# Optimization experiments

Measured on AMD Instinct MI355X. Metric: run time of the kernel, lower is better.

Reference implementation:

```python
import jax, jax.numpy as jnp
import numpy as np
import math

C = 256
GROUPS = 32
EPS = 1e-5

def setup_inputs() -> dict:
    key = jax.random.key(0)
    ks = jax.random.split(key, 11)
    B, H, W = 8, 64, 64
    s = 1.0 / math.sqrt(C)
    return {
        "x": jax.random.normal(ks[0], (B, C, H, W), dtype=jnp.float32),
        "gamma": jnp.ones((C,), jnp.float32),
        "beta": jnp.zeros((C,), jnp.float32),
        "wq": jax.random.normal(ks[1], (C, C), jnp.float32) * s,
        "bq": jnp.zeros((C,), jnp.float32),
        "wk": jax.random.normal(ks[2], (C, C), jnp.float32) * s,
        "bk": jnp.zeros((C,), jnp.float32),
        "wv": jax.random.normal(ks[3], (C, C), jnp.float32) * s,
        "bv": jnp.zeros((C,), jnp.float32),
        "wp": jax.random.normal(ks[4], (C, C), jnp.float32) * s,
        "bp": jnp.zeros((C,), jnp.float32),
    }

def _group_norm(x, gamma, beta):
    B, Cc, H, W = x.shape
    xg = x.reshape(B, GROUPS, Cc // GROUPS, H, W)
    mu = xg.mean(axis=(2, 3, 4), keepdims=True)
    var = xg.var(axis=(2, 3, 4), keepdims=True)
    xn = ((xg - mu) * jax.lax.rsqrt(var + EPS)).reshape(B, Cc, H, W)
    return xn * gamma[None, :, None, None] + beta[None, :, None, None]

def reference(x, gamma, beta, wq, bq, wk, bk, wv, bv, wp, bp):
    B, Cc, H, W = x.shape
    T = H * W
    h = _group_norm(x, gamma, beta)           # (B,C,H,W)
    hf = h.reshape(B, Cc, T)                  # (B,C,T)
    # 1x1 convs = per-pixel linear maps over channels
    q = jnp.einsum('oc,bct->bto', wq, hf) + bq           # (B,T,C)
    k = jnp.einsum('oc,bct->bot', wk, hf) + bk[:, None]  # (B,C,T)
    v = jnp.einsum('oc,bct->bto', wv, hf) + bv           # (B,T,C)
    scores = jnp.einsum('btc,bcs->bts', q, k) / math.sqrt(Cc)
    attn = jax.nn.softmax(scores, axis=-1)    # (B,T,T)
    z = jnp.einsum('bts,bsc->btc', attn, v)   # (B,T,C)
    zf = z.transpose(0, 2, 1)                 # (B,C,T)
    proj = jnp.einsum('oc,bct->bot', wp, zf) + bp[:, None]
    return x + proj.reshape(B, Cc, H, W)
```

## Files before the change

kernel.cpp:

```cpp
#include <hip/hip_runtime.h>


typedef unsigned short u16;
typedef __attribute__((ext_vector_type(8))) short short8;
typedef __attribute__((ext_vector_type(4))) float f32x4;

#define MFMA16(a, b, c) __builtin_amdgcn_mfma_f32_16x16x32_bf16((a), (b), (c), 0, 0, 0)

#define GLL16(g, l)                                                            \
  __builtin_amdgcn_global_load_lds(                                            \
      (const __attribute__((address_space(1))) void*)(g),                      \
      (__attribute__((address_space(3))) void*)(l), 16, 0, 0)

__device__ __forceinline__ u16 f2bf(float f) {
  union { float f; unsigned u; } v; v.f = f;
  unsigned u = v.u;
  return (u16)((u + 0x7FFFu + ((u >> 16) & 1u)) >> 16);
}

__global__ __launch_bounds__(256) void conv_w(const float* __restrict__ s0,
                                              const float* __restrict__ s1,
                                              const float* __restrict__ s2,
                                              const float* __restrict__ s3,
                                              u16* __restrict__ dst) {
  const int m = blockIdx.y;
  const float* s = (m == 0) ? s0 : (m == 1) ? s1 : (m == 2) ? s2 : s3;
  const int i = (blockIdx.x * 256 + threadIdx.x) * 4;
  float4 v = *(const float4*)(s + i);
  u16* d = dst + m * 65536 + i;
  d[0] = f2bf(v.x); d[1] = f2bf(v.y); d[2] = f2bf(v.z); d[3] = f2bf(v.w);
}

__global__ __launch_bounds__(256) void gn_stats(const float* __restrict__ x,
                                                float2* __restrict__ stats) {
  const int bg = blockIdx.x;
  const float* p = x + (long)bg * 32768;
  const int tid = threadIdx.x;
  float s = 0.f, ss = 0.f;
  #pragma unroll 8
  for (int i = 0; i < 32; ++i) {
    float4 v = *(const float4*)(p + tid * 4 + i * 1024);
    s  += v.x + v.y + v.z + v.w;
    ss += v.x * v.x + v.y * v.y + v.z * v.z + v.w * v.w;
  }
  for (int off = 32; off; off >>= 1) {
    s  += __shfl_down(s, off);
    ss += __shfl_down(ss, off);
  }
  __shared__ float2 red[4];
  if ((tid & 63) == 0) red[tid >> 6] = make_float2(s, ss);
  __syncthreads();
  if (tid == 0) {
    float S  = red[0].x + red[1].x + red[2].x + red[3].x;
    float SS = red[0].y + red[1].y + red[2].y + red[3].y;
    float mean = S * (1.f / 32768.f);
    float var  = SS * (1.f / 32768.f) - mean * mean;
    stats[bg] = make_float2(mean, rsqrtf(var + 1e-5f));
  }
}

__global__ __launch_bounds__(256) void gn_apply(const float* __restrict__ x,
                                                const float2* __restrict__ stats,
                                                const float* __restrict__ gamma,
                                                const float* __restrict__ beta,
                                                u16* __restrict__ h_t) {
  __shared__ float tile[64][65];
  const int tid = threadIdx.x;
  const int b = blockIdx.z, c0 = blockIdx.y * 64, t0 = blockIdx.x * 64;
  {
    const int ci = tid >> 2, tj0 = (tid & 3) * 16;
    const int c = c0 + ci;
    float2 st = stats[b * 32 + (c >> 3)];
    float gm = gamma[c] * st.y;
    float bt = beta[c] - st.x * gm;
    const float* xp = x + ((long)(b * 256 + c) * 4096 + t0 + tj0);
    #pragma unroll
    for (int i = 0; i < 4; ++i) {
      float4 v = *(const float4*)(xp + i * 4);
      tile[ci][tj0 + i * 4 + 0] = v.x * gm + bt;
      tile[ci][tj0 + i * 4 + 1] = v.y * gm + bt;
      tile[ci][tj0 + i * 4 + 2] = v.z * gm + bt;
      tile[ci][tj0 + i * 4 + 3] = v.w * gm + bt;
    }
  }
  __syncthreads();
  {
    const int tj = tid >> 2, ci0 = (tid & 3) * 16;
    u16* hp = h_t + ((long)(b * 4096 + t0 + tj) * 256 + c0 + ci0);
    short8 v0, v1;
    #pragma unroll
    for (int i = 0; i < 8; ++i) v0[i] = (short)f2bf(tile[ci0 + i][tj]);
    #pragma unroll
    for (int i = 0; i < 8; ++i) v1[i] = (short)f2bf(tile[ci0 + 8 + i][tj]);
    *(short8*)hp = v0;
    *(short8*)(hp + 8) = v1;
  }
}

template <bool ROW_BIAS, bool RESID>
__global__ __launch_bounds__(256, 2) void gemm_bt(
    const u16* __restrict__ A, long strideAz, const u16* __restrict__ B,
    long strideBz, const float* __restrict__ bias, float scale,
    u16* __restrict__ outb, float* __restrict__ outf,
    const float* __restrict__ resid, long strideOz, int N) {
  __shared__ u16 a_lds[128 * 32];
  __shared__ u16 b_lds[128 * 32];
  const int tid = threadIdx.x, w = tid >> 6, l = tid & 63;
  const int l15 = l & 15, l4 = l >> 4;
  const int bz = blockIdx.z;
  A += bz * strideAz;
  B += bz * strideBz;
  const long obase = (long)bz * strideOz;
  const int m0 = blockIdx.y * 128, n0 = blockIdx.x * 128;
  const int wm = (w >> 1) * 64, wn = (w & 1) * 64;

  f32x4 acc[4][4];
  #pragma unroll
  for (int i = 0; i < 4; ++i)
    #pragma unroll
    for (int j = 0; j < 4; ++j) acc[i][j] = (f32x4)0.f;

  for (int kt = 0; kt < 8; ++kt) {
    const int k0 = kt * 32;
    __syncthreads();
    #pragma unroll
    for (int j = 0; j < 2; ++j) {
      const int r0 = (w * 2 + j) * 16;
      const int row = r0 + (l >> 2);
      const int sg = (l & 3) ^ (row & 3);
      GLL16(A + (long)(m0 + row) * 256 + k0 + sg * 8, a_lds + r0 * 32);
      GLL16(B + (long)(n0 + row) * 256 + k0 + sg * 8, b_lds + r0 * 32);
    }
    __syncthreads();
    short8 af[4], bf[4];
    #pragma unroll
    for (int t = 0; t < 4; ++t) {
      const int ra = wm + t * 16 + l15;
      af[t] = *(const short8*)(a_lds + ra * 32 + ((l4 ^ (ra & 3)) * 8));
      const int rb = wn + t * 16 + l15;
      bf[t] = *(const short8*)(b_lds + rb * 32 + ((l4 ^ (rb & 3)) * 8));
    }
    #pragma unroll
    for (int mt = 0; mt < 4; ++mt)
      #pragma unroll
      for (int nt = 0; nt < 4; ++nt) acc[mt][nt] = MFMA16(af[mt], bf[nt], acc[mt][nt]);
  }

  if (!ROW_BIAS) {
    float bv[4];
    #pragma unroll
    for (int nt = 0; nt < 4; ++nt) bv[nt] = bias[n0 + wn + nt * 16 + l15];
    #pragma unroll
    for (int mt = 0; mt < 4; ++mt)
      #pragma unroll
      for (int nt = 0; nt < 4; ++nt)
        #pragma unroll
        for (int r = 0; r < 4; ++r) {
          const int row = m0 + wm + mt * 16 + l4 * 4 + r;
          const int col = n0 + wn + nt * 16 + l15;
          outb[obase + (long)row * N + col] = f2bf((acc[mt][nt][r] + bv[nt]) * scale);
        }
  } else {
    float bm[4][4];
    #pragma unroll
    for (int mt = 0; mt < 4; ++mt)
      #pragma unroll
      for (int r = 0; r < 4; ++r) bm[mt][r] = bias[m0 + wm + mt * 16 + l4 * 4 + r];
    #pragma unroll
    for (int mt = 0; mt < 4; ++mt)
      #pragma unroll
      for (int nt = 0; nt < 4; ++nt)
        #pragma unroll
        for (int r = 0; r < 4; ++r) {
          const int row = m0 + wm + mt * 16 + l4 * 4 + r;
          const int col = n0 + wn + nt * 16 + l15;
          const long idx = obase + (long)row * N + col;
          float v = acc[mt][nt][r] + bm[mt][r];
          if (RESID) outf[idx] = v + resid[idx];
          else       outb[idx] = f2bf(v);
        }
  }
}

__global__ __launch_bounds__(256, 2) void attn_kernel(
    const u16* __restrict__ Qs, const u16* __restrict__ Ks,
    const u16* __restrict__ Vt, u16* __restrict__ Z) {
  __shared__ u16 k_lds[16384];
  __shared__ u16 v_lds[16384];
  u16* p_lds = k_lds;
  float* l_buf = (float*)&k_lds[8192];

  const int tid = threadIdx.x, w = tid >> 6, l = tid & 63;
  const int l15 = l & 15, l4 = l >> 4;
  const int bid = blockIdx.x;
  const int batch = bid & 7;
  const int qt = bid >> 3;
  const int wrow0 = (w >> 1) * 32, wcolS = (w & 1) * 32, wcolO = (w & 1) * 128;
  const long qrow_base = (long)batch * 4096 + qt * 64;

  short8 qf[2][8];
  {
    const u16* qp = Qs + (qrow_base + wrow0) * 256;
    #pragma unroll
    for (int mt = 0; mt < 2; ++mt)
      #pragma unroll
      for (int ks = 0; ks < 8; ++ks)
        qf[mt][ks] = *(const short8*)(qp + (mt * 16 + l15) * 256 + ks * 32 + l4 * 8);
  }

  f32x4 o_acc[2][8];
  #pragma unroll
  for (int mt = 0; mt < 2; ++mt)
    #pragma unroll
    for (int nt = 0; nt < 8; ++nt) o_acc[mt][nt] = (f32x4)0.f;
  float rs[2][4] = {{0.f, 0.f, 0.f, 0.f}, {0.f, 0.f, 0.f, 0.f}};

  const u16* kbase = Ks + (long)batch * 4096 * 256;
  const u16* vbase = Vt + (long)batch * 256 * 4096;

  for (int st = 0; st < 64; ++st) {
    const int sn0 = st * 64;
    __syncthreads();
    #pragma unroll
    for (int j = 0; j < 8; ++j) {
      const int r0 = (j * 4 + w) * 2;
      const int row = r0 + (l >> 5);
      const int sg = (l & 31) ^ (row & 7);
      GLL16(kbase + (long)(sn0 + row) * 256 + sg * 8, k_lds + r0 * 256);
    }
    #pragma unroll
    for (int j = 0; j < 8; ++j) {
      const int c0 = (j * 4 + w) * 8;
      const int c = c0 + (l >> 3);
      const int sg = (l & 7) ^ (c & 7);
      GLL16(vbase + (long)c * 4096 + sn0 + sg * 8, v_lds + c0 * 64);
    }
    __syncthreads();

    f32x4 sacc[2][2];
    #pragma unroll
    for (int i = 0; i < 2; ++i)
      #pragma unroll
      for (int j = 0; j < 2; ++j) sacc[i][j] = (f32x4)0.f;
    #pragma unroll
    for (int ks = 0; ks < 8; ++ks) {
      short8 kf[2];
      #pragma unroll
      for (int nt = 0; nt < 2; ++nt) {
        const int row = wcolS + nt * 16 + l15;
        const int gk = (ks * 4 + l4) ^ (row & 7);
        kf[nt] = *(const short8*)(k_lds + row * 256 + gk * 8);
      }
      #pragma unroll
      for (int mt = 0; mt < 2; ++mt)
        #pragma unroll
        for (int nt = 0; nt < 2; ++nt) sacc[mt][nt] = MFMA16(qf[mt][ks], kf[nt], sacc[mt][nt]);
    }
    __syncthreads();

    #pragma unroll
    for (int mt = 0; mt < 2; ++mt)
      #pragma unroll
      for (int nt = 0; nt < 2; ++nt)
        #pragma unroll
        for (int r = 0; r < 4; ++r) {
          float p = __expf(sacc[mt][nt][r]);
          rs[mt][r] += p;
          const int prow = wrow0 + mt * 16 + l4 * 4 + r;
          const int pcol = wcolS + nt * 16 + l15;
          p_lds[prow * 72 + pcol] = f2bf(p);
        }
    __syncthreads();

    #pragma unroll
    for (int ks2 = 0; ks2 < 2; ++ks2) {
      short8 pa[2];
      #pragma unroll
      for (int mt = 0; mt < 2; ++mt)
        pa[mt] = *(const short8*)(p_lds + (wrow0 + mt * 16 + l15) * 72 + ks2 * 32 + l4 * 8);
      #pragma unroll
      for (int nt = 0; nt < 8; ++nt) {
        const int c = wcolO + nt * 16 + l15;
        const int gv = (ks2 * 4 + l4) ^ (c & 7);
        short8 vb = *(const short8*)(v_lds + c * 64 + gv * 8);
        #pragma unroll
        for (int mt = 0; mt < 2; ++mt) o_acc[mt][nt] = MFMA16(pa[mt], vb, o_acc[mt][nt]);
      }
    }
  }

  #pragma unroll
  for (int mt = 0; mt < 2; ++mt)
    #pragma unroll
    for (int r = 0; r < 4; ++r) {
      float v = rs[mt][r];
      v += __shfl_xor(v, 1); v += __shfl_xor(v, 2);
      v += __shfl_xor(v, 4); v += __shfl_xor(v, 8);
      rs[mt][r] = v;
    }
  if (l15 == 0) {
    #pragma unroll
    for (int mt = 0; mt < 2; ++mt)
      #pragma unroll
      for (int r = 0; r < 4; ++r)
        l_buf[(w & 1) * 64 + wrow0 + mt * 16 + l4 * 4 + r] = rs[mt][r];
  }
  __syncthreads();

  #pragma unroll
  for (int mt = 0; mt < 2; ++mt) {
    float inv[4];
    #pragma unroll
    for (int r = 0; r < 4; ++r) {
      const int row = wrow0 + mt * 16 + l4 * 4 + r;
      inv[r] = 1.f / (l_buf[row] + l_buf[64 + row]);
    }
    #pragma unroll
    for (int nt = 0; nt < 8; ++nt) {
      const int col = wcolO + nt * 16 + l15;
      #pragma unroll
      for (int r = 0; r < 4; ++r) {
        const long row = qrow_base + wrow0 + mt * 16 + l4 * 4 + r;
        Z[row * 256 + col] = f2bf(o_acc[mt][nt][r] * inv[r]);
      }
    }
  }
}

extern "C" void kernel_launch(void* const* d_in, const int* in_sizes, int n_in,
                              void* d_out, int out_size, void* d_ws, size_t ws_size,
                              hipStream_t stream) {
  (void)in_sizes; (void)n_in; (void)out_size; (void)ws_size;
  const float* x     = (const float*)d_in[0];
  const float* gamma = (const float*)d_in[1];
  const float* beta  = (const float*)d_in[2];
  const float* wq    = (const float*)d_in[3];
  const float* bq    = (const float*)d_in[4];
  const float* wk    = (const float*)d_in[5];
  const float* bk    = (const float*)d_in[6];
  const float* wv    = (const float*)d_in[7];
  const float* bv    = (const float*)d_in[8];
  const float* wp    = (const float*)d_in[9];
  const float* bp    = (const float*)d_in[10];
  float* out = (float*)d_out;

  char* ws = (char*)d_ws;
  u16*    wb    = (u16*)(ws);
  float2* stats = (float2*)(ws + 524288);
  u16*    h_t   = (u16*)(ws + 526336);
  u16*    Qs    = (u16*)(ws + 17303552);
  u16*    Ks    = (u16*)(ws + 34080768);
  u16*    Vt    = (u16*)(ws + 50857984);
  u16*    Zb    = (u16*)(ws + 67635200);

  conv_w<<<dim3(64, 4), dim3(256), 0, stream>>>(wq, wk, wv, wp, wb);
  gn_stats<<<dim3(256), dim3(256), 0, stream>>>(x, stats);
  gn_apply<<<dim3(64, 4, 8), dim3(256), 0, stream>>>(x, stats, gamma, beta, h_t);

  const long sB = 4096L * 256L, sO = 256L * 4096L;
  gemm_bt<false, false><<<dim3(2, 256, 1), dim3(256), 0, stream>>>(
      h_t, 0L, wb, 0L, bq, 0.0625f, Qs, nullptr, nullptr, 0L, 256);
  gemm_bt<false, false><<<dim3(2, 256, 1), dim3(256), 0, stream>>>(
      h_t, 0L, wb + 65536, 0L, bk, 1.0f, Ks, nullptr, nullptr, 0L, 256);
  gemm_bt<true, false><<<dim3(32, 2, 8), dim3(256), 0, stream>>>(
      wb + 2 * 65536, 0L, h_t, sB, bv, 1.0f, Vt, nullptr, nullptr, sO, 4096);

  attn_kernel<<<dim3(512), dim3(256), 0, stream>>>(Qs, Ks, Vt, Zb);

  gemm_bt<true, true><<<dim3(32, 2, 8), dim3(256), 0, stream>>>(
      wb + 3 * 65536, 0L, Zb, sB, bp, 1.0f, nullptr, out, x, sO, 4096);
}
```

Measured before the change: 320.1 us.

## Fuse Q/K projections into one GEMM and restructure attention with 32x32 MFMA

Replaces the two separate Q and K projection launches with a single gemm_qk kernel. It computes both outputs against the concatenated weight matrix, which saves a launch and reads the normalized activations once. The attention kernel is also reworked. Each wave now computes S^T for 16 keys against all 64 queries, with Q held in registers, so K fragments are loaded once per wave instead of being duplicated. The PV product moves to 32x32x16 MFMA tiles, giving larger per-instruction work and fewer LDS reads of V. P gets its own LDS buffer, which removes one barrier per tile. Register pressure rises (qf doubles to 4x8 short8, plus 64 accumulators), which risks spills or lower occupancy.

```diff
diff --git a/kernel.cpp b/kernel.cpp
--- a/kernel.cpp
+++ b/kernel.cpp
@@ -4,8 +4,10 @@
 typedef unsigned short u16;
 typedef __attribute__((ext_vector_type(8))) short short8;
 typedef __attribute__((ext_vector_type(4))) float f32x4;
+typedef __attribute__((ext_vector_type(16))) float f32x16;
 
 #define MFMA16(a, b, c) __builtin_amdgcn_mfma_f32_16x16x32_bf16((a), (b), (c), 0, 0, 0)
+#define MFMA32(a, b, c) __builtin_amdgcn_mfma_f32_32x32x16_bf16((a), (b), (c), 0, 0, 0)
 
 #define GLL16(g, l)                                                            \
   __builtin_amdgcn_global_load_lds(                                            \
@@ -182,41 +184,103 @@
   }
 }
 
+__global__ __launch_bounds__(256, 2) void gemm_qk(
+    const u16* __restrict__ A, const u16* __restrict__ Bw,
+    const float* __restrict__ bq, const float* __restrict__ bk,
+    u16* __restrict__ Qs, u16* __restrict__ Ks) {
+  __shared__ u16 a_lds[128 * 32];
+  __shared__ u16 b_lds[128 * 32];
+  const int tid = threadIdx.x, w = tid >> 6, l = tid & 63;
+  const int l15 = l & 15, l4 = l >> 4;
+  const int m0 = blockIdx.y * 128, n0 = blockIdx.x * 128;
+  const int wm = (w >> 1) * 64, wn = (w & 1) * 64;
+
+  f32x4 acc[4][4];
+  #pragma unroll
+  for (int i = 0; i < 4; ++i)
+    #pragma unroll
+    for (int j = 0; j < 4; ++j) acc[i][j] = (f32x4)0.f;
+
+  for (int kt = 0; kt < 8; ++kt) {
+    const int k0 = kt * 32;
+    __syncthreads();
+    #pragma unroll
+    for (int j = 0; j < 2; ++j) {
+      const int r0 = (w * 2 + j) * 16;
+      const int row = r0 + (l >> 2);
+      const int sg = (l & 3) ^ (row & 3);
+      GLL16(A + (long)(m0 + row) * 256 + k0 + sg * 8, a_lds + r0 * 32);
+      GLL16(Bw + (long)(n0 + row) * 256 + k0 + sg * 8, b_lds + r0 * 32);
+    }
+    __syncthreads();
+    short8 af[4], bf[4];
+    #pragma unroll
+    for (int t = 0; t < 4; ++t) {
+      const int ra = wm + t * 16 + l15;
+      af[t] = *(const short8*)(a_lds + ra * 32 + ((l4 ^ (ra & 3)) * 8));
+      const int rb = wn + t * 16 + l15;
+      bf[t] = *(const short8*)(b_lds + rb * 32 + ((l4 ^ (rb & 3)) * 8));
+    }
+    #pragma unroll
+    for (int mt = 0; mt < 4; ++mt)
+      #pragma unroll
+      for (int nt = 0; nt < 4; ++nt) acc[mt][nt] = MFMA16(af[mt], bf[nt], acc[mt][nt]);
+  }
+
+  const bool isQ = n0 < 256;
+  u16* out = isQ ? Qs : Ks;
+  const float* bias = isQ ? bq : bk;
+  const float scale = isQ ? 0.0625f : 1.0f;
+  const int nc0 = n0 & 255;
+  float bv[4];
+  #pragma unroll
+  for (int nt = 0; nt < 4; ++nt) bv[nt] = bias[nc0 + wn + nt * 16 + l15];
+  #pragma unroll
+  for (int mt = 0; mt < 4; ++mt)
+    #pragma unroll
+    for (int nt = 0; nt < 4; ++nt)
+      #pragma unroll
+      for (int r = 0; r < 4; ++r) {
+        const int row = m0 + wm + mt * 16 + l4 * 4 + r;
+        const int col = nc0 + wn + nt * 16 + l15;
+        out[(long)row * 256 + col] = f2bf((acc[mt][nt][r] + bv[nt]) * scale);
+      }
+}
+
 __global__ __launch_bounds__(256, 2) void attn_kernel(
     const u16* __restrict__ Qs, const u16* __restrict__ Ks,
     const u16* __restrict__ Vt, u16* __restrict__ Z) {
-  __shared__ u16 k_lds[16384];
-  __shared__ u16 v_lds[16384];
-  u16* p_lds = k_lds;
-  float* l_buf = (float*)&k_lds[8192];
+  __shared__ u16 k_lds[64 * 256];
+  __shared__ u16 v_lds[256 * 64];
+  __shared__ u16 p_lds[64 * 72];
+  __shared__ float l_red[256];
 
   const int tid = threadIdx.x, w = tid >> 6, l = tid & 63;
   const int l15 = l & 15, l4 = l >> 4;
+  const int l31 = l & 31, h = l >> 5;
   const int bid = blockIdx.x;
-  const int batch = bid & 7;
-  const int qt = bid >> 3;
-  const int wrow0 = (w >> 1) * 32, wcolS = (w & 1) * 32, wcolO = (w & 1) * 128;
-  const long qrow_base = (long)batch * 4096 + qt * 64;
-
-  short8 qf[2][8];
+  const int batch = bid & 7, qt64 = bid >> 3;
+  const long qrow_base = (long)batch * 4096 + qt64 * 64;
+
+  const u16* kbase = Ks + (long)batch * 4096 * 256;
+  const u16* vbase = Vt + (long)batch * 256 * 4096;
+
+  short8 qf[4][8];
   {
-    const u16* qp = Qs + (qrow_base + wrow0) * 256;
-    #pragma unroll
-    for (int mt = 0; mt < 2; ++mt)
+    const u16* qp = Qs + qrow_base * 256;
+    #pragma unroll
+    for (int mt = 0; mt < 4; ++mt)
       #pragma unroll
       for (int ks = 0; ks < 8; ++ks)
         qf[mt][ks] = *(const short8*)(qp + (mt * 16 + l15) * 256 + ks * 32 + l4 * 8);
   }
 
-  f32x4 o_acc[2][8];
-  #pragma unroll
-  for (int mt = 0; mt < 2; ++mt)
-    #pragma unroll
-    for (int nt = 0; nt < 8; ++nt) o_acc[mt][nt] = (f32x4)0.f;
-  float rs[2][4] = {{0.f, 0.f, 0.f, 0.f}, {0.f, 0.f, 0.f, 0.f}};
-
-  const u16* kbase = Ks + (long)batch * 4096 * 256;
-  const u16* vbase = Vt + (long)batch * 256 * 4096;
+  f32x16 o_acc[2][2];
+  #pragma unroll
+  for (int i = 0; i < 2; ++i)
+    #pragma unroll
+    for (int j = 0; j < 2; ++j) o_acc[i][j] = (f32x16)0.f;
+  float rs[4] = {0.f, 0.f, 0.f, 0.f};
 
   for (int st = 0; st < 64; ++st) {
     const int sn0 = st * 64;
@@ -237,94 +301,77 @@
     }
     __syncthreads();
 
-    f32x4 sacc[2][2];
-    #pragma unroll
-    for (int i = 0; i < 2; ++i)
-      #pragma unroll
-      for (int j = 0; j < 2; ++j) sacc[i][j] = (f32x4)0.f;
+    f32x4 sacc[4];
+    #pragma unroll
+    for (int mt = 0; mt < 4; ++mt) sacc[mt] = (f32x4)0.f;
+    const u16* kro = k_lds + (w * 16 + l15) * 256;
     #pragma unroll
     for (int ks = 0; ks < 8; ++ks) {
-      short8 kf[2];
-      #pragma unroll
-      for (int nt = 0; nt < 2; ++nt) {
-        const int row = wcolS + nt * 16 + l15;
-        const int gk = (ks * 4 + l4) ^ (row & 7);
-        kf[nt] = *(const short8*)(k_lds + row * 256 + gk * 8);
+      short8 kf = *(const short8*)(kro + (((ks * 4 + l4) ^ (l15 & 7)) * 8));
+      #pragma unroll
+      for (int mt = 0; mt < 4; ++mt) sacc[mt] = MFMA16(kf, qf[mt][ks], sacc[mt]);
+    }
+    #pragma unroll
+    for (int mt = 0; mt < 4; ++mt) {
+      float e0 = __expf(sacc[mt][0]), e1 = __expf(sacc[mt][1]);
+      float e2 = __expf(sacc[mt][2]), e3 = __expf(sacc[mt][3]);
+      rs[mt] += (e0 + e1) + (e2 + e3);
+      ushort4 pk = {f2bf(e0), f2bf(e1), f2bf(e2), f2bf(e3)};
+      *(ushort4*)(p_lds + (mt * 16 + l15) * 72 + w * 16 + l4 * 4) = pk;
+    }
+    __syncthreads();
+
+    #pragma unroll
+    for (int ss = 0; ss < 4; ++ss) {
+      short8 pa[2], vb[2];
+      #pragma unroll
+      for (int qt = 0; qt < 2; ++qt)
+        pa[qt] = *(const short8*)(p_lds + (qt * 32 + l31) * 72 + ss * 16 + h * 8);
+      #pragma unroll
+      for (int ct = 0; ct < 2; ++ct) {
+        const int c = w * 64 + ct * 32 + l31;
+        const int gv = (ss * 2 + h) ^ (c & 7);
+        vb[ct] = *(const short8*)(v_lds + c * 64 + gv * 8);
       }
       #pragma unroll
-      for (int mt = 0; mt < 2; ++mt)
+      for (int qt = 0; qt < 2; ++qt)
         #pragma unroll
-        for (int nt = 0; nt < 2; ++nt) sacc[mt][nt] = MFMA16(qf[mt][ks], kf[nt], sacc[mt][nt]);
-    }
-    __syncthreads();
-
-    #pragma unroll
-    for (int mt = 0; mt < 2; ++mt)
-      #pragma unroll
-      for (int nt = 0; nt < 2; ++nt)
-        #pragma unroll
-        for (int r = 0; r < 4; ++r) {
-          float p = __expf(sacc[mt][nt][r]);
-          rs[mt][r] += p;
-          const int prow = wrow0 + mt * 16 + l4 * 4 + r;
-          const int pcol = wcolS + nt * 16 + l15;
-          p_lds[prow * 72 + pcol] = f2bf(p);
-        }
-    __syncthreads();
-
-    #pragma unroll
-    for (int ks2 = 0; ks2 < 2; ++ks2) {
-      short8 pa[2];
-      #pragma unroll
-      for (int mt = 0; mt < 2; ++mt)
-        pa[mt] = *(const short8*)(p_lds + (wrow0 + mt * 16 + l15) * 72 + ks2 * 32 + l4 * 8);
-      #pragma unroll
-      for (int nt = 0; nt < 8; ++nt) {
-        const int c = wcolO + nt * 16 + l15;
-        const int gv = (ks2 * 4 + l4) ^ (c & 7);
-        short8 vb = *(const short8*)(v_lds + c * 64 + gv * 8);
-        #pragma unroll
-        for (int mt = 0; mt < 2; ++mt) o_acc[mt][nt] = MFMA16(pa[mt], vb, o_acc[mt][nt]);
+        for (int ct = 0; ct < 2; ++ct)
+          o_acc[qt][ct] = MFMA32(pa[qt], vb[ct], o_acc[qt][ct]);
+    }
+  }
+
+  #pragma unroll
+  for (int mt = 0; mt < 4; ++mt) {
+    float v = rs[mt];
+    v += __shfl_xor(v, 16);
+    v += __shfl_xor(v, 32);
+    if (l4 == 0) l_red[w * 64 + mt * 16 + l15] = v;
+  }
+  __syncthreads();
+  if (tid < 64) {
+    float t = l_red[tid] + l_red[64 + tid] + l_red[128 + tid] + l_red[192 + tid];
+    l_red[tid] = 1.f / t;
+  }
+  __syncthreads();
+
+  #pragma unroll
+  for (int qt = 0; qt < 2; ++qt)
+    #pragma unroll
+    for (int g = 0; g < 4; ++g) {
+      const int rbase = qt * 32 + 4 * h + 8 * g;
+      float i0 = l_red[rbase + 0], i1 = l_red[rbase + 1];
+      float i2 = l_red[rbase + 2], i3 = l_red[rbase + 3];
+      #pragma unroll
+      for (int ct = 0; ct < 2; ++ct) {
+        const int col = w * 64 + ct * 32 + l31;
+        u16* zp = Z + (qrow_base + rbase) * 256 + col;
+        zp[0]       = f2bf(o_acc[qt][ct][g * 4 + 0] * i0);
+        zp[256]     = f2bf(o_acc[qt][ct][g * 4 + 1] * i1);
+        zp[512]     = f2bf(o_acc[qt][ct][g * 4 + 2] * i2);
+        zp[768]     = f2bf(o_acc[qt][ct][g * 4 + 3] * i3);
       }
     }
-  }
-
-  #pragma unroll
-  for (int mt = 0; mt < 2; ++mt)
-    #pragma unroll
-    for (int r = 0; r < 4; ++r) {
-      float v = rs[mt][r];
-      v += __shfl_xor(v, 1); v += __shfl_xor(v, 2);
-      v += __shfl_xor(v, 4); v += __shfl_xor(v, 8);
-      rs[mt][r] = v;
-    }
-  if (l15 == 0) {
-    #pragma unroll
-    for (int mt = 0; mt < 2; ++mt)
-      #pragma unroll
-      for (int r = 0; r < 4; ++r)
-        l_buf[(w & 1) * 64 + wrow0 + mt * 16 + l4 * 4 + r] = rs[mt][r];
-  }
-  __syncthreads();
-
-  #pragma unroll
-  for (int mt = 0; mt < 2; ++mt) {
-    float inv[4];
-    #pragma unroll
-    for (int r = 0; r < 4; ++r) {
-      const int row = wrow0 + mt * 16 + l4 * 4 + r;
-      inv[r] = 1.f / (l_buf[row] + l_buf[64 + row]);
-    }
-    #pragma unroll
-    for (int nt = 0; nt < 8; ++nt) {
-      const int col = wcolO + nt * 16 + l15;
-      #pragma unroll
-      for (int r = 0; r < 4; ++r) {
-        const long row = qrow_base + wrow0 + mt * 16 + l4 * 4 + r;
-        Z[row * 256 + col] = f2bf(o_acc[mt][nt][r] * inv[r]);
-      }
-    }
-  }
 }
 
 extern "C" void kernel_launch(void* const* d_in, const int* in_sizes, int n_in,
@@ -358,10 +405,7 @@
   gn_apply<<<dim3(64, 4, 8), dim3(256), 0, stream>>>(x, stats, gamma, beta, h_t);
 
   const long sB = 4096L * 256L, sO = 256L * 4096L;
-  gemm_bt<false, false><<<dim3(2, 256, 1), dim3(256), 0, stream>>>(
-      h_t, 0L, wb, 0L, bq, 0.0625f, Qs, nullptr, nullptr, 0L, 256);
-  gemm_bt<false, false><<<dim3(2, 256, 1), dim3(256), 0, stream>>>(
-      h_t, 0L, wb + 65536, 0L, bk, 1.0f, Ks, nullptr, nullptr, 0L, 256);
+  gemm_qk<<<dim3(4, 256), dim3(256), 0, stream>>>(h_t, wb, bq, bk, Qs, Ks);
   gemm_bt<true, false><<<dim3(32, 2, 8), dim3(256), 0, stream>>>(
       wb + 2 * 65536, 0L, h_t, sB, bv, 1.0f, Vt, nullptr, nullptr, sO, 4096);
 
```

Result: slower. 365.6 us (+14.2%).

## Register-prefetch K/V tiles in attention and fuse Q/K projection GEMMs

Applied to the files above, without the earlier changes.

The attention kernel now loads the next K and V tiles into registers while the current tile is being computed, then writes them to LDS at the start of the following iteration. This replaces the synchronous global-to-LDS loads and drops one barrier. The P buffer gets its own LDS allocation so it no longer aliases the K tile. Separately, the Q and K projections are merged into a single GEMM launch over concatenated weights, which saves a launch and rereads of h_t. The cost is a large register footprint (16 float4 prefetch registers per thread) and more LDS use, which may reduce occupancy.

```diff
diff --git a/kernel.cpp b/kernel.cpp
--- a/kernel.cpp
+++ b/kernel.cpp
@@ -182,13 +182,76 @@
   }
 }
 
+__global__ __launch_bounds__(256, 2) void gemm_qk(
+    const u16* __restrict__ A, const u16* __restrict__ Bw,
+    const float* __restrict__ bq, const float* __restrict__ bk,
+    u16* __restrict__ Qs, u16* __restrict__ Ks) {
+  __shared__ u16 a_lds[128 * 32];
+  __shared__ u16 b_lds[128 * 32];
+  const int tid = threadIdx.x, w = tid >> 6, l = tid & 63;
+  const int l15 = l & 15, l4 = l >> 4;
+  const int m0 = blockIdx.y * 128, n0 = blockIdx.x * 128;
+  const int wm = (w >> 1) * 64, wn = (w & 1) * 64;
+
+  f32x4 acc[4][4];
+  #pragma unroll
+  for (int i = 0; i < 4; ++i)
+    #pragma unroll
+    for (int j = 0; j < 4; ++j) acc[i][j] = (f32x4)0.f;
+
+  for (int kt = 0; kt < 8; ++kt) {
+    const int k0 = kt * 32;
+    __syncthreads();
+    #pragma unroll
+    for (int j = 0; j < 2; ++j) {
+      const int r0 = (w * 2 + j) * 16;
+      const int row = r0 + (l >> 2);
+      const int sg = (l & 3) ^ (row & 3);
+      GLL16(A + (long)(m0 + row) * 256 + k0 + sg * 8, a_lds + r0 * 32);
+      GLL16(Bw + (long)(n0 + row) * 256 + k0 + sg * 8, b_lds + r0 * 32);
+    }
+    __syncthreads();
+    short8 af[4], bf[4];
+    #pragma unroll
+    for (int t = 0; t < 4; ++t) {
+      const int ra = wm + t * 16 + l15;
+      af[t] = *(const short8*)(a_lds + ra * 32 + ((l4 ^ (ra & 3)) * 8));
+      const int rb = wn + t * 16 + l15;
+      bf[t] = *(const short8*)(b_lds + rb * 32 + ((l4 ^ (rb & 3)) * 8));
+    }
+    #pragma unroll
+    for (int mt = 0; mt < 4; ++mt)
+      #pragma unroll
+      for (int nt = 0; nt < 4; ++nt) acc[mt][nt] = MFMA16(af[mt], bf[nt], acc[mt][nt]);
+  }
+
+  const bool isQ = n0 < 256;
+  u16* out = isQ ? Qs : Ks;
+  const float* bias = isQ ? bq : bk;
+  const float scale = isQ ? 0.0625f : 1.0f;
+  const int nc0 = n0 & 255;
+  float bv[4];
+  #pragma unroll
+  for (int nt = 0; nt < 4; ++nt) bv[nt] = bias[nc0 + wn + nt * 16 + l15];
+  #pragma unroll
+  for (int mt = 0; mt < 4; ++mt)
+    #pragma unroll
+    for (int nt = 0; nt < 4; ++nt)
+      #pragma unroll
+      for (int r = 0; r < 4; ++r) {
+        const int row = m0 + wm + mt * 16 + l4 * 4 + r;
+        const int col = nc0 + wn + nt * 16 + l15;
+        out[(long)row * 256 + col] = f2bf((acc[mt][nt][r] + bv[nt]) * scale);
+      }
+}
+
 __global__ __launch_bounds__(256, 2) void attn_kernel(
     const u16* __restrict__ Qs, const u16* __restrict__ Ks,
     const u16* __restrict__ Vt, u16* __restrict__ Z) {
   __shared__ u16 k_lds[16384];
   __shared__ u16 v_lds[16384];
-  u16* p_lds = k_lds;
-  float* l_buf = (float*)&k_lds[8192];
+  __shared__ u16 p_lds[64 * 72];
+  __shared__ float l_buf[128];
 
   const int tid = threadIdx.x, w = tid >> 6, l = tid & 63;
   const int l15 = l & 15, l4 = l >> 4;
@@ -198,6 +261,9 @@
   const int wrow0 = (w >> 1) * 32, wcolS = (w & 1) * 32, wcolO = (w & 1) * 128;
   const long qrow_base = (long)batch * 4096 + qt * 64;
 
+  const u16* kbase = Ks + (long)batch * 4096 * 256;
+  const u16* vbase = Vt + (long)batch * 256 * 4096;
+
   short8 qf[2][8];
   {
     const u16* qp = Qs + (qrow_base + wrow0) * 256;
@@ -208,6 +274,23 @@
         qf[mt][ks] = *(const short8*)(qp + (mt * 16 + l15) * 256 + ks * 32 + l4 * 8);
   }
 
+  const int rowk = 2 * w + (l >> 5);
+  const int sgk = (l & 31) ^ (rowk & 7);
+  const u16* kg = kbase + (long)rowk * 256 + sgk * 8;
+  const int cv = 8 * w + (l >> 3);
+  const int sgv = (l & 7) ^ (cv & 7);
+  const u16* vg = vbase + (long)cv * 4096 + sgv * 8;
+  u16* kw = k_lds + w * 512 + l * 8;
+  u16* vw = v_lds + w * 512 + l * 8;
+
+  float4 kpf[8], vpf[8];
+  #pragma unroll
+  for (int j = 0; j < 8; ++j) kpf[j] = *(const float4*)(kg + j * 2048);
+  kg += 16384;
+  #pragma unroll
+  for (int j = 0; j < 8; ++j) vpf[j] = *(const float4*)(vg + (long)j * 131072);
+  vg += 64;
+
   f32x4 o_acc[2][8];
   #pragma unroll
   for (int mt = 0; mt < 2; ++mt)
@@ -215,27 +298,19 @@
     for (int nt = 0; nt < 8; ++nt) o_acc[mt][nt] = (f32x4)0.f;
   float rs[2][4] = {{0.f, 0.f, 0.f, 0.f}, {0.f, 0.f, 0.f, 0.f}};
 
-  const u16* kbase = Ks + (long)batch * 4096 * 256;
-  const u16* vbase = Vt + (long)batch * 256 * 4096;
-
   for (int st = 0; st < 64; ++st) {
-    const int sn0 = st * 64;
-    __syncthreads();
-    #pragma unroll
-    for (int j = 0; j < 8; ++j) {
-      const int r0 = (j * 4 + w) * 2;
-      const int row = r0 + (l >> 5);
-      const int sg = (l & 31) ^ (row & 7);
-      GLL16(kbase + (long)(sn0 + row) * 256 + sg * 8, k_lds + r0 * 256);
-    }
-    #pragma unroll
-    for (int j = 0; j < 8; ++j) {
-      const int c0 = (j * 4 + w) * 8;
-      const int c = c0 + (l >> 3);
-      const int sg = (l & 7) ^ (c & 7);
-      GLL16(vbase + (long)c * 4096 + sn0 + sg * 8, v_lds + c0 * 64);
-    }
-    __syncthreads();
+    __syncthreads();
+    #pragma unroll
+    for (int j = 0; j < 8; ++j) *(float4*)(kw + j * 2048) = kpf[j];
+    #pragma unroll
+    for (int j = 0; j < 8; ++j) *(float4*)(vw + j * 2048) = vpf[j];
+    __syncthreads();
+
+    if (st < 63) {
+      #pragma unroll
+      for (int j = 0; j < 8; ++j) kpf[j] = *(const float4*)(kg + j * 2048);
+      kg += 16384;
+    }
 
     f32x4 sacc[2][2];
     #pragma unroll
@@ -256,7 +331,6 @@
         #pragma unroll
         for (int nt = 0; nt < 2; ++nt) sacc[mt][nt] = MFMA16(qf[mt][ks], kf[nt], sacc[mt][nt]);
     }
-    __syncthreads();
 
     #pragma unroll
     for (int mt = 0; mt < 2; ++mt)
@@ -271,6 +345,12 @@
           p_lds[prow * 72 + pcol] = f2bf(p);
         }
     __syncthreads();
+
+    if (st < 63) {
+      #pragma unroll
+      for (int j = 0; j < 8; ++j) vpf[j] = *(const float4*)(vg + (long)j * 131072);
+      vg += 64;
+    }
 
     #pragma unroll
     for (int ks2 = 0; ks2 < 2; ++ks2) {
@@ -358,10 +438,7 @@
   gn_apply<<<dim3(64, 4, 8), dim3(256), 0, stream>>>(x, stats, gamma, beta, h_t);
 
   const long sB = 4096L * 256L, sO = 256L * 4096L;
-  gemm_bt<false, false><<<dim3(2, 256, 1), dim3(256), 0, stream>>>(
-      h_t, 0L, wb, 0L, bq, 0.0625f, Qs, nullptr, nullptr, 0L, 256);
-  gemm_bt<false, false><<<dim3(2, 256, 1), dim3(256), 0, stream>>>(
-      h_t, 0L, wb + 65536, 0L, bk, 1.0f, Ks, nullptr, nullptr, 0L, 256);
+  gemm_qk<<<dim3(4, 256), dim3(256), 0, stream>>>(h_t, wb, bq, bk, Qs, Ks);
   gemm_bt<true, false><<<dim3(32, 2, 8), dim3(256), 0, stream>>>(
       wb + 2 * 65536, 0L, h_t, sB, bv, 1.0f, Vt, nullptr, nullptr, sO, 4096);
 
```

New measurement: 720.5 us. 125% more time.
